# Kernel tuning notes

Hardware: AMD Instinct MI355X
Metric: run time of the kernel (lower is better)

Reference implementation:

```python
import jax, jax.numpy as jnp
import numpy as np

N_NODES = 100000
N_EDGES = 3200000
IN_SIZE, HIDDEN, OUT_SIZE = 512, 16, 64


def setup_inputs() -> dict:
    key = jax.random.key(0)
    k1, k2, k3, k4, k5, k6 = jax.random.split(key, 6)
    x = jax.random.normal(k1, (N_NODES, IN_SIZE), dtype=jnp.float32)
    src = jax.random.randint(k2, (N_EDGES,), 0, N_NODES, dtype=jnp.int64)
    dst = jax.random.randint(k3, (N_EDGES,), 0, N_NODES, dtype=jnp.int64)
    # Glorot-style init like dgl GraphConv
    W1 = jax.random.normal(k4, (IN_SIZE, HIDDEN), dtype=jnp.float32) * (1.0 / np.sqrt(IN_SIZE))
    b1 = jnp.zeros((HIDDEN,), dtype=jnp.float32)
    W2 = jax.random.normal(k5, (HIDDEN, OUT_SIZE), dtype=jnp.float32) * (1.0 / np.sqrt(HIDDEN))
    b2 = jnp.zeros((OUT_SIZE,), dtype=jnp.float32)
    return {"x": x, "W1": W1, "b1": b1, "W2": W2, "b2": b2, "src": src, "dst": dst}


def _degree_norms(src, dst, n_nodes):
    ones = jnp.ones(src.shape[0], dtype=jnp.float32)
    deg_out = jnp.clip(jax.ops.segment_sum(ones, src, num_segments=n_nodes), 1.0)
    deg_in = jnp.clip(jax.ops.segment_sum(ones, dst, num_segments=n_nodes), 1.0)
    return deg_out ** -0.5, deg_in ** -0.5  # norm='both' as in dgl GraphConv


def _graph_conv(x, W, b, src, dst, norm_src, norm_dst, transform_first):
    # dgl GraphConv: applies W before aggregation when in_feats > out_feats
    h = x * norm_src[:, None]
    if transform_first:
        h = h @ W
    # SpMM: gather from src, scatter-sum to dst
    agg = jax.ops.segment_sum(h[src], dst, num_segments=x.shape[0])
    if not transform_first:
        agg = agg @ W
    return agg * norm_dst[:, None] + b


def reference(x, W1, b1, W2, b2, src, dst):
    n = x.shape[0]
    norm_src, norm_dst = _degree_norms(src, dst, n)
    h = _graph_conv(x, W1, b1, src, dst, norm_src, norm_dst, transform_first=True)  # 512>16
    h = jax.nn.relu(h)
    out = _graph_conv(h, W2, b2, src, dst, norm_src, norm_dst, transform_first=False)  # 16<64
    return out
```

## Files before the change

kernel.cpp:

```cpp
#include <hip/hip_runtime.h>

#define NT 256
#define EPB 4096
#define MAXBKT 512
#define CAP 16384

typedef __bf16 bf16x8 __attribute__((ext_vector_type(8)));
typedef float f32x4 __attribute__((ext_vector_type(4)));
typedef unsigned int u32x4 __attribute__((ext_vector_type(4)));

__device__ __forceinline__ unsigned short f2bf(float f) {
    unsigned int u = __float_as_uint(f);
    unsigned int r = u + 0x7FFFu + ((u >> 16) & 1u);
    return (unsigned short)(r >> 16);
}
__device__ __forceinline__ float bf2f(unsigned short h) {
    return __uint_as_float(((unsigned int)h) << 16);
}
__device__ __forceinline__ unsigned int pack_hi(float f0, float f1) {
    return (__float_as_uint(f0) >> 16) | (__float_as_uint(f1) & 0xFFFF0000u);
}
__device__ __forceinline__ unsigned int pack_lo(float f0, float f1) {
    float l0 = f0 - __uint_as_float(__float_as_uint(f0) & 0xFFFF0000u);
    float l1 = f1 - __uint_as_float(__float_as_uint(f1) & 0xFFFF0000u);
    return (__float_as_uint(l0) >> 16) | (__float_as_uint(l1) & 0xFFFF0000u);
}

__global__ __launch_bounds__(512) void init_w1t(int* __restrict__ gcurD,
                                                int* __restrict__ gcurS,
                                                const float* __restrict__ W1,
                                                unsigned short* __restrict__ w1t_hi,
                                                unsigned short* __restrict__ w1t_lo, int nbkt) {
    if (blockIdx.x == 0) {
        int i = threadIdx.x;
        if (i < nbkt) { gcurD[i] = i * CAP; gcurS[i] = i * CAP; }
    } else {
        int t = (blockIdx.x - 1) * 512 + threadIdx.x;
        if (t < 512 * 16) {
            int k = t >> 4, c = t & 15;
            float f = W1[k * 16 + c];
            unsigned short h = f2bf(f);
            w1t_hi[c * 512 + k] = h;
            w1t_lo[c * 512 + k] = f2bf(f - bf2f(h));
        }
    }
}

__global__ __launch_bounds__(NT) void bucket_scatter(const int* __restrict__ src,
                                                     const int* __restrict__ dst,
                                                     int* __restrict__ gcurD,
                                                     int* __restrict__ gcurS,
                                                     unsigned int* __restrict__ ebinD,
                                                     unsigned char* __restrict__ ebinS8,
                                                     int e, int nbkt) {
    __shared__ int hD[MAXBKT], hS[MAXBKT];
    __shared__ int cD[MAXBKT], cS[MAXBKT];
    int tid = threadIdx.x;
    for (int i = tid; i < nbkt; i += NT) { hD[i] = 0; hS[i] = 0; }
    __syncthreads();
    int p0 = blockIdx.x * EPB;
    int pend = min(p0 + EPB, e);
    for (int p = p0 + tid; p < pend; p += NT) {
        atomicAdd(&hD[dst[p] >> 8], 1);
        atomicAdd(&hS[src[p] >> 8], 1);
    }
    __syncthreads();
    for (int i = tid; i < nbkt; i += NT) {
        cD[i] = hD[i] ? atomicAdd(&gcurD[i], hD[i]) : 0;
        cS[i] = hS[i] ? atomicAdd(&gcurS[i], hS[i]) : 0;
    }
    __syncthreads();
    for (int p = p0 + tid; p < pend; p += NT) {
        int s = src[p], d = dst[p];
        int bd = d >> 8;
        int slotD = atomicAdd(&cD[bd], 1);
        if (slotD < (bd + 1) * CAP)
            ebinD[slotD] = (unsigned int)s | ((unsigned int)(d & 255) << 17);
        int bs = s >> 8;
        int slotS = atomicAdd(&cS[bs], 1);
        if (slotS < (bs + 1) * CAP)
            ebinS8[slotS] = (unsigned char)(s & 255);
    }
}

__global__ __launch_bounds__(NT) void src_degree(const unsigned char* __restrict__ ebinS8,
                                                 const int* __restrict__ gcurS,
                                                 float* __restrict__ norm_src, int n) {
    __shared__ int cnt[256];
    int b = blockIdx.x, tid = threadIdx.x;
    cnt[tid] = 0;
    __syncthreads();
    int p0 = b * CAP, p1 = gcurS[b];
    for (int p = p0 + tid; p < p1; p += NT) atomicAdd(&cnt[ebinS8[p]], 1);
    __syncthreads();
    int node = (b << 8) + tid;
    if (node < n) norm_src[node] = rsqrtf((float)max(cnt[tid], 1));
}

__global__ __launch_bounds__(NT) void dst_fill(const unsigned int* __restrict__ ebinD,
                                               const int* __restrict__ gcurD,
                                               int* __restrict__ rowoff,
                                               int* __restrict__ rowend,
                                               float* __restrict__ norm_dst,
                                               int* __restrict__ esrc, int n) {
    __shared__ int cnt[256], cur[256], tmp[256];
    int b = blockIdx.x, tid = threadIdx.x;
    cnt[tid] = 0;
    __syncthreads();
    int p0 = b * CAP, p1 = gcurD[b];
    for (int p = p0 + tid; p < p1; p += NT) atomicAdd(&cnt[ebinD[p] >> 17], 1);
    __syncthreads();
    int v = cnt[tid];
    int val = v;
    tmp[tid] = val;
    __syncthreads();
    for (int off = 1; off < 256; off <<= 1) {
        int a = (tid >= off) ? tmp[tid - off] : 0;
        __syncthreads();
        val += a;
        tmp[tid] = val;
        __syncthreads();
    }
    int excl = val - v;
    int node = (b << 8) + tid;
    if (node < n) {
        rowoff[node] = p0 + excl;
        rowend[node] = p0 + excl + v;
        norm_dst[node] = rsqrtf((float)max(v, 1));
    }
    cur[tid] = p0 + excl;
    __syncthreads();
    for (int p = p0 + tid; p < p1; p += NT) {
        unsigned int w = ebinD[p];
        int pos = atomicAdd(&cur[w >> 17], 1);
        esrc[pos] = (int)(w & 0x1FFFFu);
    }
}

#define GR 64
__global__ __launch_bounds__(NT) void gemm1_stream(const float* __restrict__ x,
                                                   const unsigned short* __restrict__ w1t_hi,
                                                   const unsigned short* __restrict__ w1t_lo,
                                                   const float* __restrict__ norm_src,
                                                   unsigned short* __restrict__ y1bf, int n) {
    int tid = threadIdx.x;
    int w = tid >> 6, l = tid & 63;
    int row0 = blockIdx.x * GR + w * 16;
    int r = l & 15;
    int ko = (l >> 4) * 8;
    int myrow = row0 + r;
    bool valid = myrow < n;
    const float* xrow = x + (size_t)myrow * 512;

    f32x4 acc = {0.f, 0.f, 0.f, 0.f};
#pragma unroll 2
    for (int kc = 0; kc < 512; kc += 32) {
        float4 v0 = make_float4(0.f, 0.f, 0.f, 0.f);
        float4 v1 = make_float4(0.f, 0.f, 0.f, 0.f);
        if (valid) {
            v0 = *(const float4*)&xrow[kc + ko];
            v1 = *(const float4*)&xrow[kc + ko + 4];
        }
        u32x4 H, L;
        H[0] = pack_hi(v0.x, v0.y); L[0] = pack_lo(v0.x, v0.y);
        H[1] = pack_hi(v0.z, v0.w); L[1] = pack_lo(v0.z, v0.w);
        H[2] = pack_hi(v1.x, v1.y); L[2] = pack_lo(v1.x, v1.y);
        H[3] = pack_hi(v1.z, v1.w); L[3] = pack_lo(v1.z, v1.w);
        bf16x8 a_hi = __builtin_bit_cast(bf16x8, H);
        bf16x8 a_lo = __builtin_bit_cast(bf16x8, L);
        bf16x8 b_hi = *(const bf16x8*)&w1t_hi[r * 512 + kc + ko];
        bf16x8 b_lo = *(const bf16x8*)&w1t_lo[r * 512 + kc + ko];
        acc = __builtin_amdgcn_mfma_f32_16x16x32_bf16(a_hi, b_hi, acc, 0, 0, 0);
        acc = __builtin_amdgcn_mfma_f32_16x16x32_bf16(a_lo, b_hi, acc, 0, 0, 0);
        acc = __builtin_amdgcn_mfma_f32_16x16x32_bf16(a_hi, b_lo, acc, 0, 0, 0);
    }

    int rbase = (l >> 4) * 4;
#pragma unroll
    for (int reg = 0; reg < 4; reg++) {
        int grow = row0 + rbase + reg;
        if (grow < n) y1bf[(size_t)grow * 16 + r] = f2bf(acc[reg] * norm_src[grow]);
    }
}

__global__ __launch_bounds__(NT) void aggregate_act(const unsigned short* __restrict__ feat,
                                                    const int* __restrict__ rowoff,
                                                    const int* __restrict__ rowend,
                                                    const int* __restrict__ esrc,
                                                    const float* __restrict__ norm_dst,
                                                    const float* __restrict__ norm_src,
                                                    const float* __restrict__ b1,
                                                    unsigned short* __restrict__ h1s, int n) {
    int tid = threadIdx.x;
    int d = blockIdx.x * 64 + (tid >> 2);
    int q = tid & 3;
    if (d >= n) return;
    int p = rowoff[d], end = rowend[d];
    float4 acc0 = {0.f, 0.f, 0.f, 0.f}, acc1 = {0.f, 0.f, 0.f, 0.f};
    for (; p + 4 <= end; p += 4) {
        int idx = esrc[p + q];
#pragma unroll
        for (int t = 0; t < 4; t++) {
            int s = __shfl(idx, t, 4);
            ushort4 f = *(const ushort4*)&feat[(size_t)s * 16 + q * 4];
            if (t & 1) {
                acc1.x += bf2f(f.x); acc1.y += bf2f(f.y); acc1.z += bf2f(f.z); acc1.w += bf2f(f.w);
            } else {
                acc0.x += bf2f(f.x); acc0.y += bf2f(f.y); acc0.z += bf2f(f.z); acc0.w += bf2f(f.w);
            }
        }
    }
    for (; p < end; ++p) {
        int s = esrc[p];
        ushort4 f = *(const ushort4*)&feat[(size_t)s * 16 + q * 4];
        acc0.x += bf2f(f.x); acc0.y += bf2f(f.y); acc0.z += bf2f(f.z); acc0.w += bf2f(f.w);
    }
    float nd = norm_dst[d], ns = norm_src[d];
    float4 b1v = *(const float4*)&b1[q * 4];
    ushort4 o;
    o.x = f2bf(fmaxf((acc0.x + acc1.x) * nd + b1v.x, 0.f) * ns);
    o.y = f2bf(fmaxf((acc0.y + acc1.y) * nd + b1v.y, 0.f) * ns);
    o.z = f2bf(fmaxf((acc0.z + acc1.z) * nd + b1v.z, 0.f) * ns);
    o.w = f2bf(fmaxf((acc0.w + acc1.w) * nd + b1v.w, 0.f) * ns);
    *(ushort4*)&h1s[(size_t)d * 16 + q * 4] = o;
}

__global__ __launch_bounds__(NT) void aggregate_final(const unsigned short* __restrict__ feat,
                                                      const int* __restrict__ rowoff,
                                                      const int* __restrict__ rowend,
                                                      const int* __restrict__ esrc,
                                                      const float* __restrict__ norm_dst,
                                                      const float* __restrict__ W2,
                                                      const float* __restrict__ b2,
                                                      float* __restrict__ out, int n) {
    __shared__ float sW[16 * 64];
    int tid = threadIdx.x;
#pragma unroll
    for (int i = 0; i < 4; i++) sW[tid + i * NT] = W2[tid + i * NT];
    __syncthreads();
    int d = blockIdx.x * 64 + (tid >> 2);
    int q = tid & 3;
    if (d >= n) return;
    int p = rowoff[d], end = rowend[d];
    float4 acc0 = {0.f, 0.f, 0.f, 0.f}, acc1 = {0.f, 0.f, 0.f, 0.f};
    for (; p + 4 <= end; p += 4) {
        int idx = esrc[p + q];
#pragma unroll
        for (int t = 0; t < 4; t++) {
            int s = __shfl(idx, t, 4);
            ushort4 f = *(const ushort4*)&feat[(size_t)s * 16 + q * 4];
            if (t & 1) {
                acc1.x += bf2f(f.x); acc1.y += bf2f(f.y); acc1.z += bf2f(f.z); acc1.w += bf2f(f.w);
            } else {
                acc0.x += bf2f(f.x); acc0.y += bf2f(f.y); acc0.z += bf2f(f.z); acc0.w += bf2f(f.w);
            }
        }
    }
    for (; p < end; ++p) {
        int s = esrc[p];
        ushort4 f = *(const ushort4*)&feat[(size_t)s * 16 + q * 4];
        acc0.x += bf2f(f.x); acc0.y += bf2f(f.y); acc0.z += bf2f(f.z); acc0.w += bf2f(f.w);
    }
    float4 mine;
    mine.x = acc0.x + acc1.x; mine.y = acc0.y + acc1.y;
    mine.z = acc0.z + acc1.z; mine.w = acc0.w + acc1.w;
    float a[16];
#pragma unroll
    for (int sq = 0; sq < 4; sq++) {
        a[sq * 4 + 0] = __shfl(mine.x, sq, 4);
        a[sq * 4 + 1] = __shfl(mine.y, sq, 4);
        a[sq * 4 + 2] = __shfl(mine.z, sq, 4);
        a[sq * 4 + 3] = __shfl(mine.w, sq, 4);
    }
    float nd = norm_dst[d];
    size_t ob = (size_t)d * 64 + q * 16;
#pragma unroll
    for (int j4 = 0; j4 < 4; j4++) {
        float4 bb = *(const float4*)&b2[q * 16 + j4 * 4];
        float4 o = make_float4(0.f, 0.f, 0.f, 0.f);
#pragma unroll
        for (int k = 0; k < 16; k++) {
            float ak = a[k];
            const float* wrow = &sW[k * 64 + q * 16 + j4 * 4];
            o.x += ak * wrow[0]; o.y += ak * wrow[1];
            o.z += ak * wrow[2]; o.w += ak * wrow[3];
        }
        o.x = o.x * nd + bb.x; o.y = o.y * nd + bb.y;
        o.z = o.z * nd + bb.z; o.w = o.w * nd + bb.w;
        *(float4*)&out[ob + j4 * 4] = o;
    }
}

extern "C" void kernel_launch(void* const* d_in, const int* in_sizes, int n_in,
                              void* d_out, int out_size, void* d_ws, size_t ws_size,
                              hipStream_t stream) {
    const float* x  = (const float*)d_in[0];
    const float* W1 = (const float*)d_in[1];
    const float* b1 = (const float*)d_in[2];
    const float* W2 = (const float*)d_in[3];
    const float* b2 = (const float*)d_in[4];
    const int* src  = (const int*)d_in[5];
    const int* dst  = (const int*)d_in[6];

    int n = in_sizes[0] / 512;
    int e = in_sizes[5];
    float* out = (float*)d_out;

    int nbkt = (n + 255) >> 8;

    char* ws = (char*)d_ws;
    size_t off = 0;
    auto alloc = [&](size_t bytes) { size_t o = off; off = (off + bytes + 255) & ~(size_t)255; return o; };
    int*   gcurD = (int*)(ws + alloc(MAXBKT * 4));
    int*   gcurS = (int*)(ws + alloc(MAXBKT * 4));
    float* norm_src = (float*)(ws + alloc((size_t)n * 4));
    float* norm_dst = (float*)(ws + alloc((size_t)n * 4));
    int*   rowoff   = (int*)(ws + alloc((size_t)n * 4));
    int*   rowend   = (int*)(ws + alloc((size_t)n * 4));
    unsigned int*  ebinD  = (unsigned int*)(ws + alloc((size_t)nbkt * CAP * 4));
    unsigned char* ebinS8 = (unsigned char*)(ws + alloc((size_t)nbkt * CAP));
    int*   esrc   = (int*)(ws + alloc((size_t)nbkt * CAP * 4));
    unsigned short* y1bf = (unsigned short*)(ws + alloc((size_t)n * 16 * 2));
    unsigned short* h1s  = (unsigned short*)(ws + alloc((size_t)n * 16 * 2));
    unsigned short* w1t_hi = (unsigned short*)(ws + alloc(16 * 512 * 2));
    unsigned short* w1t_lo = (unsigned short*)(ws + alloc(16 * 512 * 2));
    if (off > ws_size) return;

    int ebb = (e + EPB - 1) / EPB;
    int grb = (n + GR - 1) / GR;
    int agb = (n + 63) / 64;

    init_w1t       <<<17, 512, 0, stream>>>(gcurD, gcurS, W1, w1t_hi, w1t_lo, nbkt);
    bucket_scatter <<<ebb, NT, 0, stream>>>(src, dst, gcurD, gcurS, ebinD, ebinS8, e, nbkt);
    src_degree     <<<nbkt, NT, 0, stream>>>(ebinS8, gcurS, norm_src, n);
    gemm1_stream   <<<grb, NT, 0, stream>>>(x, w1t_hi, w1t_lo, norm_src, y1bf, n);
    dst_fill       <<<nbkt, NT, 0, stream>>>(ebinD, gcurD, rowoff, rowend, norm_dst, esrc, n);
    aggregate_act  <<<agb, NT, 0, stream>>>(y1bf, rowoff, rowend, esrc, norm_dst, norm_src, b1, h1s, n);
    aggregate_final<<<agb, NT, 0, stream>>>(h1s, rowoff, rowend, esrc, norm_dst, W2, b2, out, n);
}
```

Before: 268.5 us.

## Aggregate per dst bucket with fixed-point LDS atomics, dropping CSR build

Removes the CSR construction (dst_fill) and the src bucket pass. Source degree is now counted with direct global atomics, and both aggregation layers run one 1024-thread block per 256-node dst bucket. Each block accumulates gathered bf16 features into shared memory with integer fixed-point atomics, which keeps the sums deterministic. This cuts kernel launches and the esrc write/read traffic, but uses global atomics for degrees and quantises sums to 2^-20, which risks precision loss or overflow for large values.

```diff
diff --git a/kernel.cpp b/kernel.cpp
--- a/kernel.cpp
+++ b/kernel.cpp
@@ -4,6 +4,8 @@
 #define EPB 4096
 #define MAXBKT 512
 #define CAP 16384
+#define FPSCALE 1048576.0f
+#define FPINV   (1.0f/1048576.0f)
 
 typedef __bf16 bf16x8 __attribute__((ext_vector_type(8)));
 typedef float f32x4 __attribute__((ext_vector_type(4)));
@@ -27,13 +29,12 @@
 }
 
 __global__ __launch_bounds__(512) void init_w1t(int* __restrict__ gcurD,
-                                                int* __restrict__ gcurS,
                                                 const float* __restrict__ W1,
                                                 unsigned short* __restrict__ w1t_hi,
                                                 unsigned short* __restrict__ w1t_lo, int nbkt) {
     if (blockIdx.x == 0) {
         int i = threadIdx.x;
-        if (i < nbkt) { gcurD[i] = i * CAP; gcurS[i] = i * CAP; }
+        if (i < nbkt) gcurD[i] = i * CAP;
     } else {
         int t = (blockIdx.x - 1) * 512 + threadIdx.x;
         if (t < 512 * 16) {
@@ -46,28 +47,30 @@
     }
 }
 
+__global__ __launch_bounds__(NT) void src_degree_g(const int* __restrict__ src,
+                                                   int* __restrict__ cntS, int e) {
+    int t = blockIdx.x * NT + threadIdx.x;
+    if (t < e) atomicAdd(&cntS[src[t]], 1);
+}
+
 __global__ __launch_bounds__(NT) void bucket_scatter(const int* __restrict__ src,
                                                      const int* __restrict__ dst,
                                                      int* __restrict__ gcurD,
-                                                     int* __restrict__ gcurS,
                                                      unsigned int* __restrict__ ebinD,
-                                                     unsigned char* __restrict__ ebinS8,
                                                      int e, int nbkt) {
-    __shared__ int hD[MAXBKT], hS[MAXBKT];
-    __shared__ int cD[MAXBKT], cS[MAXBKT];
+    __shared__ int hD[MAXBKT];
+    __shared__ int cD[MAXBKT];
     int tid = threadIdx.x;
-    for (int i = tid; i < nbkt; i += NT) { hD[i] = 0; hS[i] = 0; }
+    for (int i = tid; i < nbkt; i += NT) hD[i] = 0;
     __syncthreads();
     int p0 = blockIdx.x * EPB;
     int pend = min(p0 + EPB, e);
     for (int p = p0 + tid; p < pend; p += NT) {
         atomicAdd(&hD[dst[p] >> 8], 1);
-        atomicAdd(&hS[src[p] >> 8], 1);
     }
     __syncthreads();
     for (int i = tid; i < nbkt; i += NT) {
         cD[i] = hD[i] ? atomicAdd(&gcurD[i], hD[i]) : 0;
-        cS[i] = hS[i] ? atomicAdd(&gcurS[i], hS[i]) : 0;
     }
     __syncthreads();
     for (int p = p0 + tid; p < pend; p += NT) {
@@ -76,64 +79,6 @@
         int slotD = atomicAdd(&cD[bd], 1);
         if (slotD < (bd + 1) * CAP)
             ebinD[slotD] = (unsigned int)s | ((unsigned int)(d & 255) << 17);
-        int bs = s >> 8;
-        int slotS = atomicAdd(&cS[bs], 1);
-        if (slotS < (bs + 1) * CAP)
-            ebinS8[slotS] = (unsigned char)(s & 255);
-    }
-}
-
-__global__ __launch_bounds__(NT) void src_degree(const unsigned char* __restrict__ ebinS8,
-                                                 const int* __restrict__ gcurS,
-                                                 float* __restrict__ norm_src, int n) {
-    __shared__ int cnt[256];
-    int b = blockIdx.x, tid = threadIdx.x;
-    cnt[tid] = 0;
-    __syncthreads();
-    int p0 = b * CAP, p1 = gcurS[b];
-    for (int p = p0 + tid; p < p1; p += NT) atomicAdd(&cnt[ebinS8[p]], 1);
-    __syncthreads();
-    int node = (b << 8) + tid;
-    if (node < n) norm_src[node] = rsqrtf((float)max(cnt[tid], 1));
-}
-
-__global__ __launch_bounds__(NT) void dst_fill(const unsigned int* __restrict__ ebinD,
-                                               const int* __restrict__ gcurD,
-                                               int* __restrict__ rowoff,
-                                               int* __restrict__ rowend,
-                                               float* __restrict__ norm_dst,
-                                               int* __restrict__ esrc, int n) {
-    __shared__ int cnt[256], cur[256], tmp[256];
-    int b = blockIdx.x, tid = threadIdx.x;
-    cnt[tid] = 0;
-    __syncthreads();
-    int p0 = b * CAP, p1 = gcurD[b];
-    for (int p = p0 + tid; p < p1; p += NT) atomicAdd(&cnt[ebinD[p] >> 17], 1);
-    __syncthreads();
-    int v = cnt[tid];
-    int val = v;
-    tmp[tid] = val;
-    __syncthreads();
-    for (int off = 1; off < 256; off <<= 1) {
-        int a = (tid >= off) ? tmp[tid - off] : 0;
-        __syncthreads();
-        val += a;
-        tmp[tid] = val;
-        __syncthreads();
-    }
-    int excl = val - v;
-    int node = (b << 8) + tid;
-    if (node < n) {
-        rowoff[node] = p0 + excl;
-        rowend[node] = p0 + excl + v;
-        norm_dst[node] = rsqrtf((float)max(v, 1));
-    }
-    cur[tid] = p0 + excl;
-    __syncthreads();
-    for (int p = p0 + tid; p < p1; p += NT) {
-        unsigned int w = ebinD[p];
-        int pos = atomicAdd(&cur[w >> 17], 1);
-        esrc[pos] = (int)(w & 0x1FFFFu);
     }
 }
 
@@ -141,7 +86,7 @@
 __global__ __launch_bounds__(NT) void gemm1_stream(const float* __restrict__ x,
                                                    const unsigned short* __restrict__ w1t_hi,
                                                    const unsigned short* __restrict__ w1t_lo,
-                                                   const float* __restrict__ norm_src,
+                                                   const int* __restrict__ cntS,
                                                    unsigned short* __restrict__ y1bf, int n) {
     int tid = threadIdx.x;
     int w = tid >> 6, l = tid & 63;
@@ -179,101 +124,84 @@
 #pragma unroll
     for (int reg = 0; reg < 4; reg++) {
         int grow = row0 + rbase + reg;
-        if (grow < n) y1bf[(size_t)grow * 16 + r] = f2bf(acc[reg] * norm_src[grow]);
-    }
-}
-
-__global__ __launch_bounds__(NT) void aggregate_act(const unsigned short* __restrict__ feat,
-                                                    const int* __restrict__ rowoff,
-                                                    const int* __restrict__ rowend,
-                                                    const int* __restrict__ esrc,
-                                                    const float* __restrict__ norm_dst,
-                                                    const float* __restrict__ norm_src,
-                                                    const float* __restrict__ b1,
-                                                    unsigned short* __restrict__ h1s, int n) {
-    int tid = threadIdx.x;
-    int d = blockIdx.x * 64 + (tid >> 2);
-    int q = tid & 3;
-    if (d >= n) return;
-    int p = rowoff[d], end = rowend[d];
-    float4 acc0 = {0.f, 0.f, 0.f, 0.f}, acc1 = {0.f, 0.f, 0.f, 0.f};
-    for (; p + 4 <= end; p += 4) {
-        int idx = esrc[p + q];
-#pragma unroll
-        for (int t = 0; t < 4; t++) {
-            int s = __shfl(idx, t, 4);
-            ushort4 f = *(const ushort4*)&feat[(size_t)s * 16 + q * 4];
-            if (t & 1) {
-                acc1.x += bf2f(f.x); acc1.y += bf2f(f.y); acc1.z += bf2f(f.z); acc1.w += bf2f(f.w);
-            } else {
-                acc0.x += bf2f(f.x); acc0.y += bf2f(f.y); acc0.z += bf2f(f.z); acc0.w += bf2f(f.w);
-            }
-        }
-    }
-    for (; p < end; ++p) {
-        int s = esrc[p];
-        ushort4 f = *(const ushort4*)&feat[(size_t)s * 16 + q * 4];
-        acc0.x += bf2f(f.x); acc0.y += bf2f(f.y); acc0.z += bf2f(f.z); acc0.w += bf2f(f.w);
-    }
-    float nd = norm_dst[d], ns = norm_src[d];
-    float4 b1v = *(const float4*)&b1[q * 4];
-    ushort4 o;
-    o.x = f2bf(fmaxf((acc0.x + acc1.x) * nd + b1v.x, 0.f) * ns);
-    o.y = f2bf(fmaxf((acc0.y + acc1.y) * nd + b1v.y, 0.f) * ns);
-    o.z = f2bf(fmaxf((acc0.z + acc1.z) * nd + b1v.z, 0.f) * ns);
-    o.w = f2bf(fmaxf((acc0.w + acc1.w) * nd + b1v.w, 0.f) * ns);
-    *(ushort4*)&h1s[(size_t)d * 16 + q * 4] = o;
-}
-
-__global__ __launch_bounds__(NT) void aggregate_final(const unsigned short* __restrict__ feat,
-                                                      const int* __restrict__ rowoff,
-                                                      const int* __restrict__ rowend,
-                                                      const int* __restrict__ esrc,
-                                                      const float* __restrict__ norm_dst,
-                                                      const float* __restrict__ W2,
-                                                      const float* __restrict__ b2,
-                                                      float* __restrict__ out, int n) {
+        if (grow < n) {
+            float ns = rsqrtf((float)max(cntS[grow], 1));
+            y1bf[(size_t)grow * 16 + r] = f2bf(acc[reg] * ns);
+        }
+    }
+}
+
+__global__ __launch_bounds__(1024) void agg1_int(const unsigned short* __restrict__ y1bf,
+                                                 const unsigned int* __restrict__ ebinD,
+                                                 const int* __restrict__ gcurD,
+                                                 const int* __restrict__ cntS,
+                                                 const float* __restrict__ b1,
+                                                 float* __restrict__ norm_dst,
+                                                 unsigned short* __restrict__ h1s, int n) {
+    __shared__ int acc[256][17];
+    __shared__ int cnt[256];
+    int b = blockIdx.x, tid = threadIdx.x;
+    for (int i = tid; i < 256 * 17; i += 1024) ((int*)acc)[i] = 0;
+    if (tid < 256) cnt[tid] = 0;
+    __syncthreads();
+    int p0 = b * CAP, p1 = gcurD[b];
+    int j = tid & 15;
+    for (int p = p0 + (tid >> 4); p < p1; p += 64) {
+        unsigned int w = ebinD[p];
+        int s = (int)(w & 0x1FFFFu);
+        int dl = (int)(w >> 17);
+        float v = bf2f(y1bf[(size_t)s * 16 + j]);
+        atomicAdd(&acc[dl][j], (int)rintf(v * FPSCALE));
+        if (j == 0) atomicAdd(&cnt[dl], 1);
+    }
+    __syncthreads();
+    int node0 = b << 8;
+#pragma unroll
+    for (int r = tid >> 4; r < 256; r += 64) {
+        int node = node0 + r;
+        if (node >= n) continue;
+        int c = cnt[r];
+        float nd = rsqrtf((float)max(c, 1));
+        if (j == 0) norm_dst[node] = nd;
+        float sum = (float)acc[r][j] * FPINV;
+        float ns = rsqrtf((float)max(cntS[node], 1));
+        float v = fmaxf(sum * nd + b1[j], 0.f) * ns;
+        h1s[(size_t)node * 16 + j] = f2bf(v);
+    }
+}
+
+__global__ __launch_bounds__(1024) void agg2_int(const unsigned short* __restrict__ h1s,
+                                                 const unsigned int* __restrict__ ebinD,
+                                                 const int* __restrict__ gcurD,
+                                                 const float* __restrict__ norm_dst,
+                                                 const float* __restrict__ W2,
+                                                 const float* __restrict__ b2,
+                                                 float* __restrict__ out, int n) {
+    __shared__ int acc[256][17];
     __shared__ float sW[16 * 64];
-    int tid = threadIdx.x;
-#pragma unroll
-    for (int i = 0; i < 4; i++) sW[tid + i * NT] = W2[tid + i * NT];
-    __syncthreads();
-    int d = blockIdx.x * 64 + (tid >> 2);
-    int q = tid & 3;
-    if (d >= n) return;
-    int p = rowoff[d], end = rowend[d];
-    float4 acc0 = {0.f, 0.f, 0.f, 0.f}, acc1 = {0.f, 0.f, 0.f, 0.f};
-    for (; p + 4 <= end; p += 4) {
-        int idx = esrc[p + q];
-#pragma unroll
-        for (int t = 0; t < 4; t++) {
-            int s = __shfl(idx, t, 4);
-            ushort4 f = *(const ushort4*)&feat[(size_t)s * 16 + q * 4];
-            if (t & 1) {
-                acc1.x += bf2f(f.x); acc1.y += bf2f(f.y); acc1.z += bf2f(f.z); acc1.w += bf2f(f.w);
-            } else {
-                acc0.x += bf2f(f.x); acc0.y += bf2f(f.y); acc0.z += bf2f(f.z); acc0.w += bf2f(f.w);
-            }
-        }
-    }
-    for (; p < end; ++p) {
-        int s = esrc[p];
-        ushort4 f = *(const ushort4*)&feat[(size_t)s * 16 + q * 4];
-        acc0.x += bf2f(f.x); acc0.y += bf2f(f.y); acc0.z += bf2f(f.z); acc0.w += bf2f(f.w);
-    }
-    float4 mine;
-    mine.x = acc0.x + acc1.x; mine.y = acc0.y + acc1.y;
-    mine.z = acc0.z + acc1.z; mine.w = acc0.w + acc1.w;
+    int b = blockIdx.x, tid = threadIdx.x;
+    for (int i = tid; i < 256 * 17; i += 1024) ((int*)acc)[i] = 0;
+    sW[tid] = W2[tid];
+    __syncthreads();
+    int p0 = b * CAP, p1 = gcurD[b];
+    int j = tid & 15;
+    for (int p = p0 + (tid >> 4); p < p1; p += 64) {
+        unsigned int w = ebinD[p];
+        int s = (int)(w & 0x1FFFFu);
+        int dl = (int)(w >> 17);
+        float v = bf2f(h1s[(size_t)s * 16 + j]);
+        atomicAdd(&acc[dl][j], (int)rintf(v * FPSCALE));
+    }
+    __syncthreads();
+    int node0 = b << 8;
+    int r = tid >> 2, q = tid & 3;
+    int node = node0 + r;
+    if (node >= n) return;
+    float nd = norm_dst[node];
     float a[16];
 #pragma unroll
-    for (int sq = 0; sq < 4; sq++) {
-        a[sq * 4 + 0] = __shfl(mine.x, sq, 4);
-        a[sq * 4 + 1] = __shfl(mine.y, sq, 4);
-        a[sq * 4 + 2] = __shfl(mine.z, sq, 4);
-        a[sq * 4 + 3] = __shfl(mine.w, sq, 4);
-    }
-    float nd = norm_dst[d];
-    size_t ob = (size_t)d * 64 + q * 16;
+    for (int k = 0; k < 16; k++) a[k] = (float)acc[r][k] * FPINV;
+    size_t ob = (size_t)node * 64 + q * 16;
 #pragma unroll
     for (int j4 = 0; j4 < 4; j4++) {
         float4 bb = *(const float4*)&b2[q * 16 + j4 * 4];
@@ -311,15 +239,11 @@
     char* ws = (char*)d_ws;
     size_t off = 0;
     auto alloc = [&](size_t bytes) { size_t o = off; off = (off + bytes + 255) & ~(size_t)255; return o; };
+    int*   cntS  = (int*)(ws + alloc((size_t)n * 4));
+    size_t zero_end = off;
     int*   gcurD = (int*)(ws + alloc(MAXBKT * 4));
-    int*   gcurS = (int*)(ws + alloc(MAXBKT * 4));
-    float* norm_src = (float*)(ws + alloc((size_t)n * 4));
     float* norm_dst = (float*)(ws + alloc((size_t)n * 4));
-    int*   rowoff   = (int*)(ws + alloc((size_t)n * 4));
-    int*   rowend   = (int*)(ws + alloc((size_t)n * 4));
-    unsigned int*  ebinD  = (unsigned int*)(ws + alloc((size_t)nbkt * CAP * 4));
-    unsigned char* ebinS8 = (unsigned char*)(ws + alloc((size_t)nbkt * CAP));
-    int*   esrc   = (int*)(ws + alloc((size_t)nbkt * CAP * 4));
+    unsigned int*  ebinD = (unsigned int*)(ws + alloc((size_t)nbkt * CAP * 4));
     unsigned short* y1bf = (unsigned short*)(ws + alloc((size_t)n * 16 * 2));
     unsigned short* h1s  = (unsigned short*)(ws + alloc((size_t)n * 16 * 2));
     unsigned short* w1t_hi = (unsigned short*)(ws + alloc(16 * 512 * 2));
@@ -328,13 +252,14 @@
 
     int ebb = (e + EPB - 1) / EPB;
     int grb = (n + GR - 1) / GR;
-    int agb = (n + 63) / 64;
-
-    init_w1t       <<<17, 512, 0, stream>>>(gcurD, gcurS, W1, w1t_hi, w1t_lo, nbkt);
-    bucket_scatter <<<ebb, NT, 0, stream>>>(src, dst, gcurD, gcurS, ebinD, ebinS8, e, nbkt);
-    src_degree     <<<nbkt, NT, 0, stream>>>(ebinS8, gcurS, norm_src, n);
-    gemm1_stream   <<<grb, NT, 0, stream>>>(x, w1t_hi, w1t_lo, norm_src, y1bf, n);
-    dst_fill       <<<nbkt, NT, 0, stream>>>(ebinD, gcurD, rowoff, rowend, norm_dst, esrc, n);
-    aggregate_act  <<<agb, NT, 0, stream>>>(y1bf, rowoff, rowend, esrc, norm_dst, norm_src, b1, h1s, n);
-    aggregate_final<<<agb, NT, 0, stream>>>(h1s, rowoff, rowend, esrc, norm_dst, W2, b2, out, n);
-}
+    int edb = (e + NT - 1) / NT;
+
+    hipMemsetAsync(cntS, 0, zero_end, stream);
+
+    init_w1t       <<<17, 512, 0, stream>>>(gcurD, W1, w1t_hi, w1t_lo, nbkt);
+    src_degree_g   <<<edb, NT, 0, stream>>>(src, cntS, e);
+    bucket_scatter <<<ebb, NT, 0, stream>>>(src, dst, gcurD, ebinD, e, nbkt);
+    gemm1_stream   <<<grb, NT, 0, stream>>>(x, w1t_hi, w1t_lo, cntS, y1bf, n);
+    agg1_int       <<<nbkt, 1024, 0, stream>>>(y1bf, ebinD, gcurD, cntS, b1, norm_dst, h1s, n);
+    agg2_int       <<<nbkt, 1024, 0, stream>>>(h1s, ebinD, gcurD, norm_dst, W2, b2, out, n);
+}
```

After: 438.1 us. 63.2% more time.
